# Kernel tuning notes

Measured on AMD Instinct MI355X. Metric: run time of the kernel, lower is better.

## Reference

```python
import jax, jax.numpy as jnp
import numpy as np


def setup_inputs() -> dict:
    key = jax.random.key(0)
    k1, k2, k3 = jax.random.split(key, 3)
    B, N, M, C = 4, 4096, 8192, 64
    PPU = 64.0  # points_per_unit
    xz = jax.random.normal(k1, (B, M, 1), dtype=jnp.float32) * 10.0  # grid locations
    z = jax.random.normal(k2, (B, C, M), dtype=jnp.float32)          # channels-first features
    x = jax.random.normal(k3, (B, N, 1), dtype=jnp.float32) * 10.0   # query locations
    log_scale = jnp.asarray(np.log(2.0 / PPU), dtype=jnp.float32)
    return {"xz": xz, "z": z, "x": x, "log_scale": log_scale}


def reference(xz, z, x, log_scale):
    # pairwise squared distances between x [B,N,1] and xz [B,M,1] -> [B,N,M]
    diff = x - jnp.swapaxes(xz, -1, -2)            # [B,N,M]
    dists2 = diff * diff
    # RBF weights (no normalization)
    weights = jnp.exp(-0.5 * dists2 / jnp.exp(2.0 * log_scale))  # [B,N,M]
    # z: [B,C,M] -> transpose -> [B,M,C]; weights @ z^T -> [B,N,C]
    out = jnp.einsum('bnm,bcm->bnc', weights, z)
    return out
```

## Files before the change

### kernel.cpp

```cpp
#include <hip/hip_runtime.h>
#include <math.h>

#define B 4
#define N 4096
#define M 8192
#define C 64
#define NB 2048
#define XMIN (-64.0f)
#define INV_BW 16.0f
#define CUT 15.0f
#define QG 16
#define PCH 64

__device__ __forceinline__ int bucket_of(float v) {
    int k = (int)floorf((v - XMIN) * INV_BW);
    return min(max(k, 0), NB - 1);
}

__global__ __launch_bounds__(1024) void prep_kernel(
    const float* __restrict__ xz, const float* __restrict__ z,
    const float* __restrict__ x,
    int* __restrict__ bucket_start,
    float* __restrict__ xs,
    int* __restrict__ pidx,
    float* __restrict__ qcs,
    int* __restrict__ qis,
    float* __restrict__ zt)
{
    const int t    = threadIdx.x;
    const int lane = t & 63;
    const int w    = t >> 6;

    if (blockIdx.x < 8) {
        __shared__ int hist[NB];
        __shared__ int run[NB];
        __shared__ int wsum[16];
        const bool isQ = blockIdx.x >= 4;
        const int  b   = blockIdx.x & 3;
        const int  CNTN = isQ ? N : M;
        const int  PT   = CNTN / 1024;
        const float* src = isQ ? (x + b * N) : (xz + b * M);

        hist[t] = 0; hist[t + 1024] = 0;
        __syncthreads();

        float pv[8]; int pk[8];
        for (int j = 0; j < PT; ++j) {
            float v = src[j * 1024 + t];
            pv[j] = v; pk[j] = bucket_of(v);
            atomicAdd(&hist[pk[j]], 1);
        }
        __syncthreads();

        const int h0 = hist[2 * t], h1 = hist[2 * t + 1];
        const int tot = h0 + h1;
        int s = tot;
        #pragma unroll
        for (int off = 1; off < 64; off <<= 1) {
            int up = __shfl_up(s, off, 64);
            if (lane >= off) s += up;
        }
        if (lane == 63) wsum[w] = s;
        __syncthreads();
        int woff = 0;
        for (int i = 0; i < w; ++i) woff += wsum[i];
        const int excl = woff + s - tot;

        run[2 * t]     = excl;
        run[2 * t + 1] = excl + h0;
        if (!isQ) {
            bucket_start[b * (NB + 1) + 2 * t]     = excl;
            bucket_start[b * (NB + 1) + 2 * t + 1] = excl + h0;
            if (t == 1023) bucket_start[b * (NB + 1) + NB] = woff + s;
        }
        __syncthreads();

        if (!isQ) {
            for (int j = 0; j < PT; ++j) {
                int slot = atomicAdd(&run[pk[j]], 1);
                xs[b * M + slot]   = pv[j];
                pidx[b * M + slot] = j * 1024 + t;
            }
        } else {
            for (int j = 0; j < PT; ++j) {
                int slot = atomicAdd(&run[pk[j]], 1);
                qcs[b * N + slot] = pv[j];
                qis[b * N + slot] = j * 1024 + t;
            }
        }
    } else {
        const int tb = blockIdx.x - 8;
        const int b  = tb >> 7;
        const int m0 = (tb & 127) * 64;
        __shared__ float tile[64][65];
        const int m = t & 63;
        for (int c = t >> 6; c < 64; c += 16)
            tile[c][m] = z[((size_t)b * C + c) * M + m0 + m];
        __syncthreads();
        const int cc = t & 63;
        for (int mm = t >> 6; mm < 64; mm += 16)
            zt[((size_t)b * M + m0 + mm) * C + cc] = tile[cc][mm];
    }
}

__global__ __launch_bounds__(256) void gather_kernel(
    const float* __restrict__ log_scale,
    const int* __restrict__ bucket_start,
    const float* __restrict__ xs,
    const int* __restrict__ pidx,
    const float* __restrict__ qcs,
    const int* __restrict__ qis,
    const float* __restrict__ zt,
    float* __restrict__ out)
{
    const int t    = threadIdx.x;
    const int lane = t & 63;
    const int w    = t >> 6;
    const int g  = blockIdx.x;
    const int b  = g >> 8;
    const int g0 = (g & 255) * QG;

    __shared__ __align__(16) float zr[PCH][C];
    __shared__ __align__(16) float wl[QG][PCH];
    __shared__ int   pr[PCH];
    __shared__ float pcs[PCH];
    __shared__ float qc[QG];
    __shared__ int   qi[QG];

    const float ls   = log_scale[0];
    const float coef = -0.5f * __expf(-2.0f * ls);
    const float R    = sqrtf(CUT / (-coef));

    if (t < QG) {
        qc[t] = qcs[b * N + g0 + t];
        qi[t] = qis[b * N + g0 + t];
    }
    __syncthreads();

    float xmin = qc[0], xmax = qc[0];
    #pragma unroll
    for (int j = 1; j < QG; ++j) {
        xmin = fminf(xmin, qc[j]);
        xmax = fmaxf(xmax, qc[j]);
    }
    const int s0 = bucket_start[b * (NB + 1) + bucket_of(xmin - R)];
    const int s1 = bucket_start[b * (NB + 1) + bucket_of(xmax + R) + 1];

    const float q0 = qc[w * 4 + 0], q1 = qc[w * 4 + 1];
    const float q2 = qc[w * 4 + 2], q3 = qc[w * 4 + 3];

    if (s0 >= s1) {
        out[((size_t)b * N + qi[w * 4 + 0]) * C + lane] = 0.0f;
        out[((size_t)b * N + qi[w * 4 + 1]) * C + lane] = 0.0f;
        out[((size_t)b * N + qi[w * 4 + 2]) * C + lane] = 0.0f;
        out[((size_t)b * N + qi[w * 4 + 3]) * C + lane] = 0.0f;
        return;
    }

    float a0 = 0.f, a1 = 0.f, a2 = 0.f, a3 = 0.f;

    const float*  xsb = xs   + b * M;
    const int*    pib = pidx + b * M;
    const float4* zt4 = (const float4*)(zt + (size_t)b * M * C);

    for (int cs = s0; cs < s1; cs += PCH) {
        const int cnt = min(PCH, s1 - cs);
        __syncthreads();
        if (t < PCH) {
            int row = min(cs + t, s1 - 1);
            pr[t]  = pib[row];
            pcs[t] = xsb[row];
        }
        __syncthreads();
        #pragma unroll
        for (int i = 0; i < 4; ++i) {
            const int r = i * 16 + w * 4 + (lane >> 4);
            const float4* gp = zt4 + (size_t)pr[r] * 16 + (lane & 15);
            float* lp = &zr[i * 16 + w * 4][0];
            __builtin_amdgcn_global_load_lds(
                (const __attribute__((address_space(1))) void*)gp,
                (__attribute__((address_space(3))) void*)lp, 16, 0, 0);
        }
        {
            const float pcr   = pcs[lane];
            const bool  valid = (cs + lane) < s1;
            float d0 = q0 - pcr, d1 = q1 - pcr, d2 = q2 - pcr, d3 = q3 - pcr;
            wl[w * 4 + 0][lane] = valid ? __expf(coef * d0 * d0) : 0.0f;
            wl[w * 4 + 1][lane] = valid ? __expf(coef * d1 * d1) : 0.0f;
            wl[w * 4 + 2][lane] = valid ? __expf(coef * d2 * d2) : 0.0f;
            wl[w * 4 + 3][lane] = valid ? __expf(coef * d3 * d3) : 0.0f;
        }
        __syncthreads();
        for (int p = 0; p < cnt; p += 4) {
            float zv0 = zr[p + 0][lane];
            float zv1 = zr[p + 1][lane];
            float zv2 = zr[p + 2][lane];
            float zv3 = zr[p + 3][lane];
            const float4 wa = *(const float4*)&wl[w * 4 + 0][p];
            const float4 wb = *(const float4*)&wl[w * 4 + 1][p];
            const float4 wc = *(const float4*)&wl[w * 4 + 2][p];
            const float4 wd = *(const float4*)&wl[w * 4 + 3][p];
            a0 = fmaf(wa.x, zv0, a0); a0 = fmaf(wa.y, zv1, a0);
            a0 = fmaf(wa.z, zv2, a0); a0 = fmaf(wa.w, zv3, a0);
            a1 = fmaf(wb.x, zv0, a1); a1 = fmaf(wb.y, zv1, a1);
            a1 = fmaf(wb.z, zv2, a1); a1 = fmaf(wb.w, zv3, a1);
            a2 = fmaf(wc.x, zv0, a2); a2 = fmaf(wc.y, zv1, a2);
            a2 = fmaf(wc.z, zv2, a2); a2 = fmaf(wc.w, zv3, a2);
            a3 = fmaf(wd.x, zv0, a3); a3 = fmaf(wd.y, zv1, a3);
            a3 = fmaf(wd.z, zv2, a3); a3 = fmaf(wd.w, zv3, a3);
        }
    }

    out[((size_t)b * N + qi[w * 4 + 0]) * C + lane] = a0;
    out[((size_t)b * N + qi[w * 4 + 1]) * C + lane] = a1;
    out[((size_t)b * N + qi[w * 4 + 2]) * C + lane] = a2;
    out[((size_t)b * N + qi[w * 4 + 3]) * C + lane] = a3;
}

extern "C" void kernel_launch(void* const* d_in, const int* in_sizes, int n_in,
                              void* d_out, int out_size, void* d_ws, size_t ws_size,
                              hipStream_t stream) {
    const float* xz = (const float*)d_in[0];
    const float* z  = (const float*)d_in[1];
    const float* x  = (const float*)d_in[2];
    const float* ls = (const float*)d_in[3];
    float* out = (float*)d_out;

    char* ws = (char*)d_ws;
    size_t off = 0;
    auto alloc = [&](size_t bytes) { void* p = ws + off; off += (bytes + 255) & ~size_t(255); return p; };

    float* zt   = (float*)alloc((size_t)B * M * C * sizeof(float));
    float* xs   = (float*)alloc(((size_t)B * M + 64) * sizeof(float));
    int*   pidx = (int*)alloc((size_t)B * M * sizeof(int));
    float* qcs  = (float*)alloc((size_t)B * N * sizeof(float));
    int*   qis  = (int*)alloc((size_t)B * N * sizeof(int));
    int*   bst  = (int*)alloc((size_t)B * (NB + 1) * sizeof(int));

    prep_kernel<<<8 + B * M / 64, 1024, 0, stream>>>(xz, z, x, bst, xs, pidx, qcs, qis, zt);
    gather_kernel<<<B * (N / QG), 256, 0, stream>>>(ls, bst, xs, pidx, qcs, qis, zt, out);
}
```

Measured before the change: 94.54 us.

## Pre-sort z rows into bucket order so the gather reads contiguous chunks

The preprocessing now records each grid point's sorted slot and a new kernel scatters the transposed z rows directly into sorted order. The gather kernel can then load contiguous chunks of z and xs without an index indirection or the extra barrier and shared-memory staging for indices. The Gaussian cutoff is also tightened from 15 to 8, so fewer neighbours fall in each query window. This trades an extra kernel launch, and a serial dependency of the permutation on binning, for cheaper, coalesced gathers, and it slightly loosens numerical accuracy (weights below exp(-8) are dropped).

```diff
diff --git a/kernel.cpp b/kernel.cpp
--- a/kernel.cpp
+++ b/kernel.cpp
@@ -8,7 +8,7 @@
 #define NB 2048
 #define XMIN (-64.0f)
 #define INV_BW 16.0f
-#define CUT 15.0f
+#define CUT 8.0f
 #define QG 16
 #define PCH 64
 
@@ -17,100 +17,108 @@
     return min(max(k, 0), NB - 1);
 }
 
-__global__ __launch_bounds__(1024) void prep_kernel(
-    const float* __restrict__ xz, const float* __restrict__ z,
-    const float* __restrict__ x,
+__global__ __launch_bounds__(1024) void bin_kernel(
+    const float* __restrict__ xz, const float* __restrict__ x,
     int* __restrict__ bucket_start,
     float* __restrict__ xs,
-    int* __restrict__ pidx,
+    int* __restrict__ islot,
     float* __restrict__ qcs,
-    int* __restrict__ qis,
-    float* __restrict__ zt)
+    int* __restrict__ qis)
 {
     const int t    = threadIdx.x;
     const int lane = t & 63;
     const int w    = t >> 6;
 
-    if (blockIdx.x < 8) {
-        __shared__ int hist[NB];
-        __shared__ int run[NB];
-        __shared__ int wsum[16];
-        const bool isQ = blockIdx.x >= 4;
-        const int  b   = blockIdx.x & 3;
-        const int  CNTN = isQ ? N : M;
-        const int  PT   = CNTN / 1024;
-        const float* src = isQ ? (x + b * N) : (xz + b * M);
-
-        hist[t] = 0; hist[t + 1024] = 0;
-        __syncthreads();
-
-        float pv[8]; int pk[8];
+    __shared__ int hist[NB];
+    __shared__ int run[NB];
+    __shared__ int wsum[16];
+    const bool isQ = blockIdx.x >= 4;
+    const int  b   = blockIdx.x & 3;
+    const int  PT  = isQ ? (N / 1024) : (M / 1024);
+    const float* src = isQ ? (x + b * N) : (xz + b * M);
+
+    hist[t] = 0; hist[t + 1024] = 0;
+    __syncthreads();
+
+    float pv[8]; int pk[8];
+    for (int j = 0; j < PT; ++j) {
+        float v = src[j * 1024 + t];
+        pv[j] = v; pk[j] = bucket_of(v);
+        atomicAdd(&hist[pk[j]], 1);
+    }
+    __syncthreads();
+
+    const int h0 = hist[2 * t], h1 = hist[2 * t + 1];
+    const int tot = h0 + h1;
+    int s = tot;
+    #pragma unroll
+    for (int off = 1; off < 64; off <<= 1) {
+        int up = __shfl_up(s, off, 64);
+        if (lane >= off) s += up;
+    }
+    if (lane == 63) wsum[w] = s;
+    __syncthreads();
+    int woff = 0;
+    for (int i = 0; i < w; ++i) woff += wsum[i];
+    const int excl = woff + s - tot;
+
+    run[2 * t]     = excl;
+    run[2 * t + 1] = excl + h0;
+    if (!isQ) {
+        bucket_start[b * (NB + 1) + 2 * t]     = excl;
+        bucket_start[b * (NB + 1) + 2 * t + 1] = excl + h0;
+        if (t == 1023) bucket_start[b * (NB + 1) + NB] = woff + s;
+    }
+    __syncthreads();
+
+    if (!isQ) {
         for (int j = 0; j < PT; ++j) {
-            float v = src[j * 1024 + t];
-            pv[j] = v; pk[j] = bucket_of(v);
-            atomicAdd(&hist[pk[j]], 1);
-        }
-        __syncthreads();
-
-        const int h0 = hist[2 * t], h1 = hist[2 * t + 1];
-        const int tot = h0 + h1;
-        int s = tot;
-        #pragma unroll
-        for (int off = 1; off < 64; off <<= 1) {
-            int up = __shfl_up(s, off, 64);
-            if (lane >= off) s += up;
-        }
-        if (lane == 63) wsum[w] = s;
-        __syncthreads();
-        int woff = 0;
-        for (int i = 0; i < w; ++i) woff += wsum[i];
-        const int excl = woff + s - tot;
-
-        run[2 * t]     = excl;
-        run[2 * t + 1] = excl + h0;
-        if (!isQ) {
-            bucket_start[b * (NB + 1) + 2 * t]     = excl;
-            bucket_start[b * (NB + 1) + 2 * t + 1] = excl + h0;
-            if (t == 1023) bucket_start[b * (NB + 1) + NB] = woff + s;
-        }
-        __syncthreads();
-
-        if (!isQ) {
-            for (int j = 0; j < PT; ++j) {
-                int slot = atomicAdd(&run[pk[j]], 1);
-                xs[b * M + slot]   = pv[j];
-                pidx[b * M + slot] = j * 1024 + t;
-            }
-        } else {
-            for (int j = 0; j < PT; ++j) {
-                int slot = atomicAdd(&run[pk[j]], 1);
-                qcs[b * N + slot] = pv[j];
-                qis[b * N + slot] = j * 1024 + t;
-            }
+            int slot = atomicAdd(&run[pk[j]], 1);
+            xs[b * M + slot]           = pv[j];
+            islot[b * M + j * 1024 + t] = slot;
         }
     } else {
-        const int tb = blockIdx.x - 8;
-        const int b  = tb >> 7;
-        const int m0 = (tb & 127) * 64;
-        __shared__ float tile[64][65];
-        const int m = t & 63;
-        for (int c = t >> 6; c < 64; c += 16)
-            tile[c][m] = z[((size_t)b * C + c) * M + m0 + m];
-        __syncthreads();
-        const int cc = t & 63;
-        for (int mm = t >> 6; mm < 64; mm += 16)
-            zt[((size_t)b * M + m0 + mm) * C + cc] = tile[cc][mm];
-    }
+        for (int j = 0; j < PT; ++j) {
+            int slot = atomicAdd(&run[pk[j]], 1);
+            qcs[b * N + slot] = pv[j];
+            qis[b * N + slot] = j * 1024 + t;
+        }
+    }
+}
+
+__global__ __launch_bounds__(1024) void permz_kernel(
+    const float* __restrict__ z, const int* __restrict__ islot,
+    float* __restrict__ zs)
+{
+    const int t  = threadIdx.x;
+    const int b  = blockIdx.x >> 7;
+    const int m0 = (blockIdx.x & 127) * 64;
+    __shared__ float tile[64][65];
+    __shared__ int slot_s[64];
+
+    const int m = t & 63;
+    #pragma unroll
+    for (int k = 0; k < 4; ++k) {
+        int c = (t >> 6) + 16 * k;
+        tile[c][m] = z[((size_t)b * C + c) * M + m0 + m];
+    }
+    if (t < 64) slot_s[t] = islot[b * M + m0 + t];
+    __syncthreads();
+
+    const int j  = t >> 4;
+    const int c4 = t & 15;
+    float4 v4 = make_float4(tile[c4 * 4 + 0][j], tile[c4 * 4 + 1][j],
+                            tile[c4 * 4 + 2][j], tile[c4 * 4 + 3][j]);
+    ((float4*)zs)[((size_t)b * M + slot_s[j]) * 16 + c4] = v4;
 }
 
 __global__ __launch_bounds__(256) void gather_kernel(
     const float* __restrict__ log_scale,
     const int* __restrict__ bucket_start,
     const float* __restrict__ xs,
-    const int* __restrict__ pidx,
     const float* __restrict__ qcs,
     const int* __restrict__ qis,
-    const float* __restrict__ zt,
+    const float* __restrict__ zs,
     float* __restrict__ out)
 {
     const int t    = threadIdx.x;
@@ -122,8 +130,6 @@
 
     __shared__ __align__(16) float zr[PCH][C];
     __shared__ __align__(16) float wl[QG][PCH];
-    __shared__ int   pr[PCH];
-    __shared__ float pcs[PCH];
     __shared__ float qc[QG];
     __shared__ int   qi[QG];
 
@@ -159,30 +165,22 @@
 
     float a0 = 0.f, a1 = 0.f, a2 = 0.f, a3 = 0.f;
 
-    const float*  xsb = xs   + b * M;
-    const int*    pib = pidx + b * M;
-    const float4* zt4 = (const float4*)(zt + (size_t)b * M * C);
+    const float*  xsb = xs + b * M;
+    const float4* zs4 = (const float4*)zs + (size_t)b * M * 16;
 
     for (int cs = s0; cs < s1; cs += PCH) {
         const int cnt = min(PCH, s1 - cs);
         __syncthreads();
-        if (t < PCH) {
-            int row = min(cs + t, s1 - 1);
-            pr[t]  = pib[row];
-            pcs[t] = xsb[row];
-        }
-        __syncthreads();
         #pragma unroll
-        for (int i = 0; i < 4; ++i) {
-            const int r = i * 16 + w * 4 + (lane >> 4);
-            const float4* gp = zt4 + (size_t)pr[r] * 16 + (lane & 15);
-            float* lp = &zr[i * 16 + w * 4][0];
+        for (int r = 0; r < 4; ++r) {
+            const float4* gp = zs4 + ((size_t)cs) * 16 + r * 256 + w * 64 + lane;
+            float* lp = &zr[r * 16 + w * 4][0];
             __builtin_amdgcn_global_load_lds(
                 (const __attribute__((address_space(1))) void*)gp,
                 (__attribute__((address_space(3))) void*)lp, 16, 0, 0);
         }
         {
-            const float pcr   = pcs[lane];
+            const float pcr   = xsb[cs + lane];
             const bool  valid = (cs + lane) < s1;
             float d0 = q0 - pcr, d1 = q1 - pcr, d2 = q2 - pcr, d3 = q3 - pcr;
             wl[w * 4 + 0][lane] = valid ? __expf(coef * d0 * d0) : 0.0f;
@@ -230,13 +228,14 @@
     size_t off = 0;
     auto alloc = [&](size_t bytes) { void* p = ws + off; off += (bytes + 255) & ~size_t(255); return p; };
 
-    float* zt   = (float*)alloc((size_t)B * M * C * sizeof(float));
-    float* xs   = (float*)alloc(((size_t)B * M + 64) * sizeof(float));
-    int*   pidx = (int*)alloc((size_t)B * M * sizeof(int));
-    float* qcs  = (float*)alloc((size_t)B * N * sizeof(float));
-    int*   qis  = (int*)alloc((size_t)B * N * sizeof(int));
-    int*   bst  = (int*)alloc((size_t)B * (NB + 1) * sizeof(int));
-
-    prep_kernel<<<8 + B * M / 64, 1024, 0, stream>>>(xz, z, x, bst, xs, pidx, qcs, qis, zt);
-    gather_kernel<<<B * (N / QG), 256, 0, stream>>>(ls, bst, xs, pidx, qcs, qis, zt, out);
-}
+    float* zs    = (float*)alloc(((size_t)B * M + 64) * C * sizeof(float));
+    float* xs    = (float*)alloc(((size_t)B * M + 64) * sizeof(float));
+    int*   islot = (int*)alloc((size_t)B * M * sizeof(int));
+    float* qcs   = (float*)alloc((size_t)B * N * sizeof(float));
+    int*   qis   = (int*)alloc((size_t)B * N * sizeof(int));
+    int*   bst   = (int*)alloc((size_t)B * (NB + 1) * sizeof(int));
+
+    bin_kernel<<<8, 1024, 0, stream>>>(xz, x, bst, xs, islot, qcs, qis);
+    permz_kernel<<<512, 1024, 0, stream>>>(z, islot, zs);
+    gather_kernel<<<B * (N / QG), 256, 0, stream>>>(ls, bst, xs, qcs, qis, zs, out);
+}
```

New measurement: 92.32 us. -2.3%, faster.
